# Performance work log

Hardware: AMD Instinct MI355X
Metric: run time of the kernel (lower is better)

## Reference

```python
import jax, jax.numpy as jnp
import numpy as np
import math

B, LQ, LK = 4, 1024, 2048
QD, KD, VD = 768, 512, 512
H, NH = 1024, 16
HD = H // NH

def setup_inputs() -> dict:
    key = jax.random.key(0)
    ks = jax.random.split(key, 11)
    s = 0.02
    return {
        "query": jax.random.normal(ks[0], (B, LQ, QD), jnp.float32),
        "key": jax.random.normal(ks[1], (B, LK, KD), jnp.float32),
        "value": jax.random.normal(ks[2], (B, LK, VD), jnp.float32),
        "Wq": jax.random.normal(ks[3], (QD, H), jnp.float32) * s,
        "bq": jnp.zeros((H,), jnp.float32),
        "Wk": jax.random.normal(ks[4], (KD, H), jnp.float32) * s,
        "bk": jnp.zeros((H,), jnp.float32),
        "Wv": jax.random.normal(ks[5], (VD, H), jnp.float32) * s,
        "bv": jnp.zeros((H,), jnp.float32),
        "Wo": jax.random.normal(ks[6], (H, H), jnp.float32) * s,
        "bo": jnp.zeros((H,), jnp.float32),
    }

def reference(query, key, value, Wq, bq, Wk, bk, Wv, bv, Wo, bo):
    # project and split heads: [B, L, H] -> [B, NH, L, HD]
    def heads(x):
        b, l, _ = x.shape
        return x.reshape(b, l, NH, HD).transpose(0, 2, 1, 3)
    q = heads(query @ Wq + bq)   # [B, NH, LQ, HD]
    k = heads(key @ Wk + bk)     # [B, NH, LK, HD]
    v = heads(value @ Wv + bv)   # [B, NH, LK, HD]
    scores = jnp.einsum('bhqd,bhkd->bhqk', q, k) / math.sqrt(HD)
    weights = jax.nn.softmax(scores, axis=-1)  # dropout inactive (eval / rate used deterministically as identity)
    att = jnp.einsum('bhqk,bhkd->bhqd', weights, v)
    att = att.transpose(0, 2, 1, 3).reshape(query.shape[0], -1, H)
    out = att @ Wo + bo
    return out
```

## Files before the change

kernel.cpp:

```cpp
#include <hip/hip_runtime.h>
#include <math.h>

using bf16x8 = __attribute__((ext_vector_type(8))) short;
using f32x4  = __attribute__((ext_vector_type(4))) float;
using u32x2  = __attribute__((ext_vector_type(2))) unsigned int;

namespace {
constexpr int kB  = 4;
constexpr int kLQ = 1024;
constexpr int kLK = 2048;
constexpr int kH  = 1024;
constexpr int kHD = 64;
}

__device__ __forceinline__ unsigned short f2bf(float x) {
  union { float f; unsigned int u; } v; v.f = x;
  unsigned int r = v.u + 0x7fffu + ((v.u >> 16) & 1u);
  return (unsigned short)(r >> 16);
}

typedef const __attribute__((address_space(1))) unsigned int guint_t;
typedef __attribute__((address_space(3))) unsigned int luint_t;
__device__ __forceinline__ void g2l16(const void* g, void* l) {
  __builtin_amdgcn_global_load_lds(
      (guint_t*)g,
      (luint_t*)(unsigned int)(unsigned long long)l,
      16, 0, 0);
}

__global__ __launch_bounds__(256) void prep_kernel(
    const float* __restrict__ q, const float* __restrict__ k,
    const float* __restrict__ v, const float* __restrict__ Wq,
    const float* __restrict__ Wk, const float* __restrict__ Wv,
    const float* __restrict__ Wo, unsigned short* __restrict__ qo,
    unsigned short* __restrict__ ko, unsigned short* __restrict__ vo,
    unsigned short* __restrict__ WqT, unsigned short* __restrict__ WkT,
    unsigned short* __restrict__ WvT, unsigned short* __restrict__ WoT)
{
  __shared__ float tile[64][65];
  const int t = threadIdx.x;
  if (blockIdx.x < 5632) {
    int c = blockIdx.x * 256 + t;
    const float* src; unsigned short* dst;
    if (c < 393216)      { src = q; dst = qo; }
    else if (c < 917504) { src = k; dst = ko; c -= 393216; }
    else                 { src = v; dst = vo; c -= 917504; }
    const int i = c * 8;
    const float4 a = *(const float4*)(src + i);
    const float4 b = *(const float4*)(src + i + 4);
    uint4 o;
    o.x = (unsigned int)f2bf(a.x) | ((unsigned int)f2bf(a.y) << 16);
    o.y = (unsigned int)f2bf(a.z) | ((unsigned int)f2bf(a.w) << 16);
    o.z = (unsigned int)f2bf(b.x) | ((unsigned int)f2bf(b.y) << 16);
    o.w = (unsigned int)f2bf(b.z) | ((unsigned int)f2bf(b.w) << 16);
    *(uint4*)(dst + i) = o;
    return;
  }
  int id = blockIdx.x - 5632;
  const float* W; unsigned short* Wt; int Kd;
  if (id < 192)      { W = Wq; Wt = WqT; Kd = 768; }
  else if (id < 320) { W = Wk; Wt = WkT; Kd = 512;  id -= 192; }
  else if (id < 448) { W = Wv; Wt = WvT; Kd = 512;  id -= 320; }
  else               { W = Wo; Wt = WoT; Kd = 1024; id -= 448; }
  const int Nd = 1024;
  const int n0 = (id & 15) * 64;
  const int k0 = (id >> 4) * 64;
  const int rr = t >> 4;
  const int c4 = t & 15;
#pragma unroll
  for (int i = 0; i < 4; ++i) {
    const int row = i * 16 + rr;
    const float4 vv = *(const float4*)(W + (size_t)(k0 + row) * Nd + n0 + c4 * 4);
    tile[row][c4*4+0] = vv.x; tile[row][c4*4+1] = vv.y;
    tile[row][c4*4+2] = vv.z; tile[row][c4*4+3] = vv.w;
  }
  __syncthreads();
#pragma unroll
  for (int i = 0; i < 4; ++i) {
    const int n = i * 16 + rr;
    ushort4 o;
    o.x = f2bf(tile[c4*4+0][n]); o.y = f2bf(tile[c4*4+1][n]);
    o.z = f2bf(tile[c4*4+2][n]); o.w = f2bf(tile[c4*4+3][n]);
    *(ushort4*)(Wt + (size_t)(n0 + n) * Kd + k0 + c4 * 4) = o;
  }
}

__device__ __forceinline__ void gemm_body(
    const unsigned short* __restrict__ A, const unsigned short* __restrict__ Bt,
    const float* __restrict__ bias, void* __restrict__ Cout,
    int N, int K, int bx, int by, int mode, float scale, char* lds)
{
  const int t    = threadIdx.x;
  const int lane = t & 63;
  const int w    = t >> 6;
  const int l15  = lane & 15;
  const int lq8  = (lane >> 4) * 8;
  const int lq4  = (lane >> 4) * 4;
  const int r0   = by * 128;
  const int c0   = bx * 128;
  const int wm   = w >> 1, wn = w & 1;

  f32x4 acc[4][4] = {};

  const unsigned short* gsrc[4];
  char* ldst[4];
#pragma unroll
  for (int i = 0; i < 4; ++i) {
    const int g = w * 4 + i;
    const unsigned short* src = (g < 8) ? A : Bt;
    const int rbase = (g < 8) ? (r0 + g * 16) : (c0 + (g - 8) * 16);
    gsrc[i] = src + (size_t)(rbase + l15) * K + lq8;
    ldst[i] = lds + g * 1024 + lane * 16;
  }

#pragma unroll
  for (int i = 0; i < 4; ++i) g2l16(gsrc[i], ldst[i]);
#pragma unroll
  for (int i = 0; i < 4; ++i) g2l16(gsrc[i] + 32, ldst[i] + 16384);

  int slot = 0;
  for (int k0 = 0; k0 < K; k0 += 32) {
    if (k0 + 32 < K) {
      asm volatile("s_waitcnt vmcnt(4)\n\ts_barrier" ::: "memory");
    } else {
      asm volatile("s_waitcnt vmcnt(0)\n\ts_barrier" ::: "memory");
    }
    char* buf = lds + slot * 16384;
    if (k0 + 64 < K) {
      int ns = slot + 2; if (ns >= 3) ns -= 3;
#pragma unroll
      for (int i = 0; i < 4; ++i)
        g2l16(gsrc[i] + k0 + 64, ldst[i] + ns * 16384);
    }
    bf16x8 af[4], bfr[4];
#pragma unroll
    for (int i = 0; i < 4; ++i) af[i]  = *(const bf16x8*)(buf + (wm*4 + i) * 1024 + lane * 16);
#pragma unroll
    for (int j = 0; j < 4; ++j) bfr[j] = *(const bf16x8*)(buf + 8192 + (wn*4 + j) * 1024 + lane * 16);
#pragma unroll
    for (int i = 0; i < 4; ++i)
#pragma unroll
      for (int j = 0; j < 4; ++j)
        acc[i][j] = (mode == 2)
          ? __builtin_amdgcn_mfma_f32_16x16x32_bf16(af[i], bfr[j], acc[i][j], 0, 0, 0)
          : __builtin_amdgcn_mfma_f32_16x16x32_bf16(bfr[j], af[i], acc[i][j], 0, 0, 0);
    slot = (slot == 2) ? 0 : slot + 1;
  }

  if (mode == 2) {
#pragma unroll
    for (int j = 0; j < 4; ++j) {
      const int col = c0 + wn * 64 + j * 16 + l15;
      const float bcol = bias[col];
#pragma unroll
      for (int i = 0; i < 4; ++i) {
        const int row = r0 + wm * 64 + i * 16 + lq4;
        unsigned short* out = (unsigned short*)Cout;
        const int bb = row >> 11;
        const int lk = row & 2047;
        ushort4 o;
        o.x = f2bf(acc[i][j][0] + bcol); o.y = f2bf(acc[i][j][1] + bcol);
        o.z = f2bf(acc[i][j][2] + bcol); o.w = f2bf(acc[i][j][3] + bcol);
        *(ushort4*)(out + (size_t)(bb * kH + col) * kLK + lk) = o;
      }
    }
  } else {
#pragma unroll
    for (int i = 0; i < 4; ++i) {
      const int row = r0 + wm * 64 + i * 16 + l15;
#pragma unroll
      for (int j = 0; j < 4; ++j) {
        const int ncol = c0 + wn * 64 + j * 16 + lq4;
        const float4 b4 = *(const float4*)(bias + ncol);
        if (mode == 0) {
          float4 o;
          o.x = acc[i][j][0] + b4.x; o.y = acc[i][j][1] + b4.y;
          o.z = acc[i][j][2] + b4.z; o.w = acc[i][j][3] + b4.w;
          *(float4*)((float*)Cout + (size_t)row * N + ncol) = o;
        } else {
          ushort4 o;
          o.x = f2bf((acc[i][j][0] + b4.x) * scale);
          o.y = f2bf((acc[i][j][1] + b4.y) * scale);
          o.z = f2bf((acc[i][j][2] + b4.z) * scale);
          o.w = f2bf((acc[i][j][3] + b4.w) * scale);
          *(ushort4*)((unsigned short*)Cout + (size_t)row * N + ncol) = o;
        }
      }
    }
  }
}

__global__ __launch_bounds__(256) void qkv_gemm_kernel(
    const unsigned short* __restrict__ qA, const unsigned short* __restrict__ WqT,
    const float* __restrict__ bq, unsigned short* __restrict__ Qb,
    const unsigned short* __restrict__ kA, const unsigned short* __restrict__ WkT,
    const float* __restrict__ bk, unsigned short* __restrict__ Kb,
    const unsigned short* __restrict__ vA, const unsigned short* __restrict__ WvT,
    const float* __restrict__ bv, unsigned short* __restrict__ Vtw)
{
  __shared__ __align__(16) char lds[49152];
  int id = blockIdx.x;
  if (id < 256) {
    gemm_body(qA, WqT, bq, Qb, 1024, 768, id & 7, id >> 3, 1,
              0.18033688011112042f, lds);
  } else if (id < 768) {
    id -= 256;
    gemm_body(kA, WkT, bk, Kb, 1024, 512, id & 7, id >> 3, 1, 1.f, lds);
  } else {
    id -= 768;
    gemm_body(vA, WvT, bv, Vtw, 1024, 512, id & 7, id >> 3, 2, 1.f, lds);
  }
}

__global__ __launch_bounds__(256) void out_gemm_kernel(
    const unsigned short* __restrict__ A, const unsigned short* __restrict__ Bt,
    const float* __restrict__ bias, float* __restrict__ C)
{
  __shared__ __align__(16) char lds[49152];
  const int id = blockIdx.x;
  gemm_body(A, Bt, bias, C, 1024, 1024, id & 7, id >> 3, 0, 1.f, lds);
}

__global__ __launch_bounds__(512) void attn_mfma_kernel(
    const unsigned short* __restrict__ Q, const unsigned short* __restrict__ K,
    const unsigned short* __restrict__ Vt, unsigned short* __restrict__ O)
{
  __shared__ __align__(16) char lds[49152];
  constexpr int POFF = 32768;
  const int t    = threadIdx.x;
  const int lane = t & 63;
  const int w    = t >> 6;
  const int l15  = lane & 15;
  const int lg   = lane >> 4;
  const int lq8  = lg * 8;
  const int lq4  = lg * 4;
  const int flat = blockIdx.x;
  const int bh   = flat & 63;
  const int qb   = flat >> 6;
  const int h    = bh & 15;
  const int b    = bh >> 4;
  const int q0   = qb * 128;
  const int hoff = h * kHD;
  constexpr int NT = kLK / 64;

  bf16x8 qf[2];
#pragma unroll
  for (int kh = 0; kh < 2; ++kh)
    qf[kh] = *(const bf16x8*)(Q + (size_t)(b*kLQ + q0 + w*16 + l15) * kH
                                + hoff + kh*32 + lq8);

  f32x4 acc[4] = {};
  float lsum = 0.f;

  const int swz  = ((l15 * 5) & 7) << 4;
  const int colw = (lg * 8)  ^ swz;
  const int colr = (lg * 16) ^ swz;
  char* const prow = lds + POFF + (w*16 + l15) * 128;

  const unsigned short* gsrc[2];
  int gstep[2];
  char* ldst[2];
#pragma unroll
  for (int i = 0; i < 2; ++i) {
    const int g = w * 2 + i;
    if (g < 8) {
      gsrc[i]  = K + (size_t)(b*kLK + (g >> 1)*16 + l15) * kH + hoff + (g & 1)*32 + lq8;
      gstep[i] = 64 * kH;
    } else {
      const int gg = g - 8;
      gsrc[i]  = Vt + (size_t)(b*kH + hoff + (gg >> 1)*16 + l15) * kLK + (gg & 1)*32 + lq8;
      gstep[i] = 64;
    }
    ldst[i] = lds + g * 1024 + lane * 16;
  }

  g2l16(gsrc[0], ldst[0]);
  g2l16(gsrc[1], ldst[1]);

  for (int kt = 0; kt < NT; ++kt) {
    asm volatile("s_waitcnt vmcnt(0)\n\ts_barrier" ::: "memory");
    char* buf = lds + (kt & 1) * 16384;
    if (kt + 1 < NT) {
      const int ns = (kt + 1) & 1;
      g2l16(gsrc[0] + (size_t)(kt + 1) * gstep[0], ldst[0] + ns * 16384);
      g2l16(gsrc[1] + (size_t)(kt + 1) * gstep[1], ldst[1] + ns * 16384);
    }

    f32x4 s[4];
#pragma unroll
    for (int kcf = 0; kcf < 4; ++kcf) {
      const bf16x8 kf0 = *(const bf16x8*)(buf + (kcf*2 + 0) * 1024 + lane * 16);
      const bf16x8 kf1 = *(const bf16x8*)(buf + (kcf*2 + 1) * 1024 + lane * 16);
      f32x4 z = {};
      z = __builtin_amdgcn_mfma_f32_16x16x32_bf16(kf0, qf[0], z, 0, 0, 0);
      z = __builtin_amdgcn_mfma_f32_16x16x32_bf16(kf1, qf[1], z, 0, 0, 0);
      s[kcf] = z;
    }

#pragma unroll
    for (int kcf = 0; kcf < 4; ++kcf) {
      const float p0 = __builtin_amdgcn_exp2f(s[kcf][0]);
      const float p1 = __builtin_amdgcn_exp2f(s[kcf][1]);
      const float p2 = __builtin_amdgcn_exp2f(s[kcf][2]);
      const float p3 = __builtin_amdgcn_exp2f(s[kcf][3]);
      lsum += (p0 + p1) + (p2 + p3);
      u32x2 pw;
      pw.x = __builtin_amdgcn_perm(__float_as_uint(p1), __float_as_uint(p0), 0x07060302u);
      pw.y = __builtin_amdgcn_perm(__float_as_uint(p3), __float_as_uint(p2), 0x07060302u);
      *(u32x2*)(prow + (colw ^ (kcf * 32))) = pw;
    }

    bf16x8 pf[2];
#pragma unroll
    for (int kq = 0; kq < 2; ++kq)
      pf[kq] = *(const bf16x8*)(prow + (colr ^ (kq * 64)));
#pragma unroll
    for (int vd = 0; vd < 4; ++vd) {
      const bf16x8 vf0 = *(const bf16x8*)(buf + 8192 + (vd*2 + 0) * 1024 + lane * 16);
      const bf16x8 vf1 = *(const bf16x8*)(buf + 8192 + (vd*2 + 1) * 1024 + lane * 16);
      acc[vd] = __builtin_amdgcn_mfma_f32_16x16x32_bf16(vf0, pf[0], acc[vd], 0, 0, 0);
      acc[vd] = __builtin_amdgcn_mfma_f32_16x16x32_bf16(vf1, pf[1], acc[vd], 0, 0, 0);
    }
  }

  float v = lsum;
  v += __shfl_xor(v, 16);
  v += __shfl_xor(v, 32);
  const float rinv = 1.f / v;
#pragma unroll
  for (int vd = 0; vd < 4; ++vd) {
    ushort4 o;
    o.x = f2bf(acc[vd][0] * rinv);
    o.y = f2bf(acc[vd][1] * rinv);
    o.z = f2bf(acc[vd][2] * rinv);
    o.w = f2bf(acc[vd][3] * rinv);
    *(ushort4*)(O + (size_t)(b*kLQ + q0 + w*16 + l15) * kH
                  + hoff + vd*16 + lq4) = o;
  }
}

extern "C" void kernel_launch(void* const* d_in, const int* in_sizes, int n_in,
                              void* d_out, int out_size, void* d_ws, size_t ws_size,
                              hipStream_t stream) {
  (void)in_sizes; (void)n_in; (void)out_size; (void)ws_size;
  const float* query = (const float*)d_in[0];
  const float* key   = (const float*)d_in[1];
  const float* value = (const float*)d_in[2];
  const float* Wq = (const float*)d_in[3];
  const float* bq = (const float*)d_in[4];
  const float* Wk = (const float*)d_in[5];
  const float* bk = (const float*)d_in[6];
  const float* Wv = (const float*)d_in[7];
  const float* bv = (const float*)d_in[8];
  const float* Wo = (const float*)d_in[9];
  const float* bo = (const float*)d_in[10];
  float* out = (float*)d_out;

  unsigned short* ws  = (unsigned short*)d_ws;
  unsigned short* qA  = ws;
  unsigned short* kA  = qA  + 3145728;
  unsigned short* vA  = kA  + 4194304;
  unsigned short* WqT = vA  + 4194304;
  unsigned short* WkT = WqT + 786432;
  unsigned short* WvT = WkT + 524288;
  unsigned short* WoT = WvT + 524288;
  unsigned short* Qb  = WoT + 1048576;
  unsigned short* Kb  = Qb  + 4194304;
  unsigned short* Vtw = Kb  + 8388608;
  unsigned short* Ab  = Vtw + 8388608;

  prep_kernel<<<6336, 256, 0, stream>>>(query, key, value, Wq, Wk, Wv, Wo,
                                        qA, kA, vA, WqT, WkT, WvT, WoT);
  qkv_gemm_kernel<<<1280, 256, 0, stream>>>(qA, WqT, bq, Qb,
                                            kA, WkT, bk, Kb,
                                            vA, WvT, bv, Vtw);
  attn_mfma_kernel<<<512, 512, 0, stream>>>(Qb, Kb, Vtw, Ab);
  out_gemm_kernel<<<256, 256, 0, stream>>>(Ab, WoT, bo, out);
}
```

Before: 225.4 us.

## Fuse fp32-to-bf16 activation conversion into QKV GEMM operand loading

The separate conversion pass that turned query/key/value into bf16 copies is removed. In the QKV GEMM, waves 0-1 now load fp32 A tiles through registers, pack them to bf16 and write them to LDS with a register prefetch. Waves 2-3 keep the async global-to-LDS path for the weight tiles. This avoids writing and re-reading the bf16 activation copies, but it makes the A-loading waves synchronous and uneven, which can stall the MFMA pipeline.

```diff
diff --git a/kernel.cpp b/kernel.cpp
--- a/kernel.cpp
+++ b/kernel.cpp
@@ -17,6 +17,17 @@
   union { float f; unsigned int u; } v; v.f = x;
   unsigned int r = v.u + 0x7fffu + ((v.u >> 16) & 1u);
   return (unsigned short)(r >> 16);
+}
+
+__device__ __forceinline__ unsigned int pk2(float a, float b) {
+  return (unsigned int)f2bf(a) | ((unsigned int)f2bf(b) << 16);
+}
+
+__device__ __forceinline__ uint4 pack8(const float4& a, const float4& b) {
+  uint4 o;
+  o.x = pk2(a.x, a.y); o.y = pk2(a.z, a.w);
+  o.z = pk2(b.x, b.y); o.w = pk2(b.z, b.w);
+  return o;
 }
 
 typedef const __attribute__((address_space(1))) unsigned int guint_t;
@@ -29,34 +40,14 @@
 }
 
 __global__ __launch_bounds__(256) void prep_kernel(
-    const float* __restrict__ q, const float* __restrict__ k,
-    const float* __restrict__ v, const float* __restrict__ Wq,
-    const float* __restrict__ Wk, const float* __restrict__ Wv,
-    const float* __restrict__ Wo, unsigned short* __restrict__ qo,
-    unsigned short* __restrict__ ko, unsigned short* __restrict__ vo,
+    const float* __restrict__ Wq, const float* __restrict__ Wk,
+    const float* __restrict__ Wv, const float* __restrict__ Wo,
     unsigned short* __restrict__ WqT, unsigned short* __restrict__ WkT,
     unsigned short* __restrict__ WvT, unsigned short* __restrict__ WoT)
 {
   __shared__ float tile[64][65];
   const int t = threadIdx.x;
-  if (blockIdx.x < 5632) {
-    int c = blockIdx.x * 256 + t;
-    const float* src; unsigned short* dst;
-    if (c < 393216)      { src = q; dst = qo; }
-    else if (c < 917504) { src = k; dst = ko; c -= 393216; }
-    else                 { src = v; dst = vo; c -= 917504; }
-    const int i = c * 8;
-    const float4 a = *(const float4*)(src + i);
-    const float4 b = *(const float4*)(src + i + 4);
-    uint4 o;
-    o.x = (unsigned int)f2bf(a.x) | ((unsigned int)f2bf(a.y) << 16);
-    o.y = (unsigned int)f2bf(a.z) | ((unsigned int)f2bf(a.w) << 16);
-    o.z = (unsigned int)f2bf(b.x) | ((unsigned int)f2bf(b.y) << 16);
-    o.w = (unsigned int)f2bf(b.z) | ((unsigned int)f2bf(b.w) << 16);
-    *(uint4*)(dst + i) = o;
-    return;
-  }
-  int id = blockIdx.x - 5632;
+  int id = blockIdx.x;
   const float* W; unsigned short* Wt; int Kd;
   if (id < 192)      { W = Wq; Wt = WqT; Kd = 768; }
   else if (id < 320) { W = Wk; Wt = WkT; Kd = 512;  id -= 192; }
@@ -85,8 +76,9 @@
   }
 }
 
+template<bool AFP32>
 __device__ __forceinline__ void gemm_body(
-    const unsigned short* __restrict__ A, const unsigned short* __restrict__ Bt,
+    const void* Ain, const unsigned short* __restrict__ Bt,
     const float* __restrict__ bias, void* __restrict__ Cout,
     int N, int K, int bx, int by, int mode, float scale, char* lds)
 {
@@ -102,36 +94,7 @@
 
   f32x4 acc[4][4] = {};
 
-  const unsigned short* gsrc[4];
-  char* ldst[4];
-#pragma unroll
-  for (int i = 0; i < 4; ++i) {
-    const int g = w * 4 + i;
-    const unsigned short* src = (g < 8) ? A : Bt;
-    const int rbase = (g < 8) ? (r0 + g * 16) : (c0 + (g - 8) * 16);
-    gsrc[i] = src + (size_t)(rbase + l15) * K + lq8;
-    ldst[i] = lds + g * 1024 + lane * 16;
-  }
-
-#pragma unroll
-  for (int i = 0; i < 4; ++i) g2l16(gsrc[i], ldst[i]);
-#pragma unroll
-  for (int i = 0; i < 4; ++i) g2l16(gsrc[i] + 32, ldst[i] + 16384);
-
-  int slot = 0;
-  for (int k0 = 0; k0 < K; k0 += 32) {
-    if (k0 + 32 < K) {
-      asm volatile("s_waitcnt vmcnt(4)\n\ts_barrier" ::: "memory");
-    } else {
-      asm volatile("s_waitcnt vmcnt(0)\n\ts_barrier" ::: "memory");
-    }
-    char* buf = lds + slot * 16384;
-    if (k0 + 64 < K) {
-      int ns = slot + 2; if (ns >= 3) ns -= 3;
-#pragma unroll
-      for (int i = 0; i < 4; ++i)
-        g2l16(gsrc[i] + k0 + 64, ldst[i] + ns * 16384);
-    }
+  auto compute = [&](char* buf) {
     bf16x8 af[4], bfr[4];
 #pragma unroll
     for (int i = 0; i < 4; ++i) af[i]  = *(const bf16x8*)(buf + (wm*4 + i) * 1024 + lane * 16);
@@ -144,7 +107,136 @@
         acc[i][j] = (mode == 2)
           ? __builtin_amdgcn_mfma_f32_16x16x32_bf16(af[i], bfr[j], acc[i][j], 0, 0, 0)
           : __builtin_amdgcn_mfma_f32_16x16x32_bf16(bfr[j], af[i], acc[i][j], 0, 0, 0);
-    slot = (slot == 2) ? 0 : slot + 1;
+  };
+
+  if constexpr (!AFP32) {
+    const unsigned short* A = (const unsigned short*)Ain;
+    const unsigned short* gsrc[4];
+    char* ldst[4];
+#pragma unroll
+    for (int i = 0; i < 4; ++i) {
+      const int g = w * 4 + i;
+      const unsigned short* src = (g < 8) ? A : Bt;
+      const int rbase = (g < 8) ? (r0 + g * 16) : (c0 + (g - 8) * 16);
+      gsrc[i] = src + (size_t)(rbase + l15) * K + lq8;
+      ldst[i] = lds + g * 1024 + lane * 16;
+    }
+#pragma unroll
+    for (int i = 0; i < 4; ++i) g2l16(gsrc[i], ldst[i]);
+#pragma unroll
+    for (int i = 0; i < 4; ++i) g2l16(gsrc[i] + 32, ldst[i] + 16384);
+    int slot = 0;
+    for (int k0 = 0; k0 < K; k0 += 32) {
+      if (k0 + 32 < K) {
+        asm volatile("s_waitcnt vmcnt(4)\n\ts_barrier" ::: "memory");
+      } else {
+        asm volatile("s_waitcnt vmcnt(0)\n\ts_barrier" ::: "memory");
+      }
+      char* buf = lds + slot * 16384;
+      if (k0 + 64 < K) {
+        int ns = slot + 2; if (ns >= 3) ns -= 3;
+#pragma unroll
+        for (int i = 0; i < 4; ++i)
+          g2l16(gsrc[i] + k0 + 64, ldst[i] + ns * 16384);
+      }
+      compute(buf);
+      slot = (slot == 2) ? 0 : slot + 1;
+    }
+  } else {
+    const int NT = K / 32;
+    if (w < 2) {
+      const float* fsrc[4];
+      char* adst[4];
+#pragma unroll
+      for (int i = 0; i < 4; ++i) {
+        const int g = w * 4 + i;
+        fsrc[i] = (const float*)Ain + (size_t)(r0 + g * 16 + l15) * K + lq8;
+        adst[i] = lds + g * 1024 + lane * 16;
+      }
+      float4 sA[8], sB[8];
+#pragma unroll
+      for (int i = 0; i < 4; ++i) {
+        sA[2*i]   = *(const float4*)(fsrc[i]);
+        sA[2*i+1] = *(const float4*)(fsrc[i] + 4);
+      }
+#pragma unroll
+      for (int i = 0; i < 4; ++i)
+        *(uint4*)(adst[i]) = pack8(sA[2*i], sA[2*i+1]);
+#pragma unroll
+      for (int i = 0; i < 4; ++i) {
+        sB[2*i]   = *(const float4*)(fsrc[i] + 32);
+        sB[2*i+1] = *(const float4*)(fsrc[i] + 36);
+      }
+      int slot = 0;
+      for (int kt = 0; kt < NT; kt += 2) {
+        asm volatile("s_waitcnt lgkmcnt(0)\n\ts_barrier" ::: "memory");
+        {
+          char* buf = lds + slot * 16384;
+          if (kt + 2 < NT) {
+#pragma unroll
+            for (int i = 0; i < 4; ++i) {
+              sA[2*i]   = *(const float4*)(fsrc[i] + (kt + 2) * 32);
+              sA[2*i+1] = *(const float4*)(fsrc[i] + (kt + 2) * 32 + 4);
+            }
+          }
+          const int wo = ((slot == 2) ? 0 : slot + 1) * 16384;
+#pragma unroll
+          for (int i = 0; i < 4; ++i)
+            *(uint4*)(adst[i] + wo) = pack8(sB[2*i], sB[2*i+1]);
+          compute(buf);
+          slot = (slot == 2) ? 0 : slot + 1;
+        }
+        asm volatile("s_waitcnt lgkmcnt(0)\n\ts_barrier" ::: "memory");
+        {
+          char* buf = lds + slot * 16384;
+          if (kt + 3 < NT) {
+#pragma unroll
+            for (int i = 0; i < 4; ++i) {
+              sB[2*i]   = *(const float4*)(fsrc[i] + (kt + 3) * 32);
+              sB[2*i+1] = *(const float4*)(fsrc[i] + (kt + 3) * 32 + 4);
+            }
+          }
+          if (kt + 2 < NT) {
+            const int wo = ((slot == 2) ? 0 : slot + 1) * 16384;
+#pragma unroll
+            for (int i = 0; i < 4; ++i)
+              *(uint4*)(adst[i] + wo) = pack8(sA[2*i], sA[2*i+1]);
+          }
+          compute(buf);
+          slot = (slot == 2) ? 0 : slot + 1;
+        }
+      }
+    } else {
+      const unsigned short* gsrc[4];
+      char* ldst[4];
+#pragma unroll
+      for (int i = 0; i < 4; ++i) {
+        const int g = (w - 2) * 4 + i;
+        gsrc[i] = Bt + (size_t)(c0 + g * 16 + l15) * K + lq8;
+        ldst[i] = lds + 8192 + g * 1024 + lane * 16;
+      }
+#pragma unroll
+      for (int i = 0; i < 4; ++i) g2l16(gsrc[i], ldst[i]);
+#pragma unroll
+      for (int i = 0; i < 4; ++i) g2l16(gsrc[i] + 32, ldst[i] + 16384);
+      int slot = 0;
+      for (int k0 = 0; k0 < K; k0 += 32) {
+        if (k0 + 32 < K) {
+          asm volatile("s_waitcnt vmcnt(4)\n\ts_barrier" ::: "memory");
+        } else {
+          asm volatile("s_waitcnt vmcnt(0)\n\ts_barrier" ::: "memory");
+        }
+        char* buf = lds + slot * 16384;
+        if (k0 + 64 < K) {
+          int ns = slot + 2; if (ns >= 3) ns -= 3;
+#pragma unroll
+          for (int i = 0; i < 4; ++i)
+            g2l16(gsrc[i] + k0 + 64, ldst[i] + ns * 16384);
+        }
+        compute(buf);
+        slot = (slot == 2) ? 0 : slot + 1;
+      }
+    }
   }
 
   if (mode == 2) {
@@ -191,24 +283,24 @@
 }
 
 __global__ __launch_bounds__(256) void qkv_gemm_kernel(
-    const unsigned short* __restrict__ qA, const unsigned short* __restrict__ WqT,
+    const float* __restrict__ query, const unsigned short* __restrict__ WqT,
     const float* __restrict__ bq, unsigned short* __restrict__ Qb,
-    const unsigned short* __restrict__ kA, const unsigned short* __restrict__ WkT,
+    const float* __restrict__ key, const unsigned short* __restrict__ WkT,
     const float* __restrict__ bk, unsigned short* __restrict__ Kb,
-    const unsigned short* __restrict__ vA, const unsigned short* __restrict__ WvT,
+    const float* __restrict__ value, const unsigned short* __restrict__ WvT,
     const float* __restrict__ bv, unsigned short* __restrict__ Vtw)
 {
   __shared__ __align__(16) char lds[49152];
   int id = blockIdx.x;
   if (id < 256) {
-    gemm_body(qA, WqT, bq, Qb, 1024, 768, id & 7, id >> 3, 1,
-              0.18033688011112042f, lds);
+    gemm_body<true>(query, WqT, bq, Qb, 1024, 768, id & 7, id >> 3, 1,
+                    0.18033688011112042f, lds);
   } else if (id < 768) {
     id -= 256;
-    gemm_body(kA, WkT, bk, Kb, 1024, 512, id & 7, id >> 3, 1, 1.f, lds);
+    gemm_body<true>(key, WkT, bk, Kb, 1024, 512, id & 7, id >> 3, 1, 1.f, lds);
   } else {
     id -= 768;
-    gemm_body(vA, WvT, bv, Vtw, 1024, 512, id & 7, id >> 3, 2, 1.f, lds);
+    gemm_body<true>(value, WvT, bv, Vtw, 1024, 512, id & 7, id >> 3, 2, 1.f, lds);
   }
 }
 
@@ -218,7 +310,7 @@
 {
   __shared__ __align__(16) char lds[49152];
   const int id = blockIdx.x;
-  gemm_body(A, Bt, bias, C, 1024, 1024, id & 7, id >> 3, 0, 1.f, lds);
+  gemm_body<false>(A, Bt, bias, C, 1024, 1024, id & 7, id >> 3, 0, 1.f, lds);
 }
 
 __global__ __launch_bounds__(512) void attn_mfma_kernel(
@@ -357,10 +449,7 @@
   float* out = (float*)d_out;
 
   unsigned short* ws  = (unsigned short*)d_ws;
-  unsigned short* qA  = ws;
-  unsigned short* kA  = qA  + 3145728;
-  unsigned short* vA  = kA  + 4194304;
-  unsigned short* WqT = vA  + 4194304;
+  unsigned short* WqT = ws;
   unsigned short* WkT = WqT + 786432;
   unsigned short* WvT = WkT + 524288;
   unsigned short* WoT = WvT + 524288;
@@ -369,11 +458,10 @@
   unsigned short* Vtw = Kb  + 8388608;
   unsigned short* Ab  = Vtw + 8388608;
 
-  prep_kernel<<<6336, 256, 0, stream>>>(query, key, value, Wq, Wk, Wv, Wo,
-                                        qA, kA, vA, WqT, WkT, WvT, WoT);
-  qkv_gemm_kernel<<<1280, 256, 0, stream>>>(qA, WqT, bq, Qb,
-                                            kA, WkT, bk, Kb,
-                                            vA, WvT, bv, Vtw);
+  prep_kernel<<<704, 256, 0, stream>>>(Wq, Wk, Wv, Wo, WqT, WkT, WvT, WoT);
+  qkv_gemm_kernel<<<1280, 256, 0, stream>>>(query, WqT, bq, Qb,
+                                            key, WkT, bk, Kb,
+                                            value, WvT, bv, Vtw);
   attn_mfma_kernel<<<512, 512, 0, stream>>>(Qb, Kb, Vtw, Ab);
   out_gemm_kernel<<<256, 256, 0, stream>>>(Ab, WoT, bo, out);
 }
```

After: 272.5 us. 20.9% more time.
